# Kernel tuning notes

Measured on AMD Instinct MI355X. Metric: run time of the kernel, lower is better.

Reference implementation:

```python
import jax, jax.numpy as jnp
import numpy as np

B, C, H, W = 8, 4, 96, 96
HW = H * W
DIST = 320.0 ** 2  # ctor default normalizer
INF = 1e10


def _edge_mask(img, pad_val):
    # img: [H, W]. 4-neighbor sum with out-of-bounds value pad_val
    # (pad_val=1 for background channel 0, else 0), matching torch F.pad usage.
    row = jnp.full((1, W), pad_val, img.dtype)
    col = jnp.full((H, 1), pad_val, img.dtype)
    below = jnp.concatenate([img[1:, :], row], axis=0)   # neighbor below
    above = jnp.concatenate([row, img[:-1, :]], axis=0)  # neighbor above
    right = jnp.concatenate([img[:, 1:], col], axis=1)   # neighbor right
    left = jnp.concatenate([col, img[:, :-1]], axis=1)   # neighbor left
    edge = jnp.clip(4.0 * img - (below + above + right + left), 0.0, 1.0)
    return edge > 0  # nonzero() selection as boolean mask over pixels


def _pairwise_sqdist_table():
    # D[p, g] = squared euclidean distance between pixel coords p and g. [HW, HW]
    dy = (jnp.arange(H, dtype=jnp.float32)[:, None] - jnp.arange(H, dtype=jnp.float32)[None, :]) ** 2
    dx = (jnp.arange(W, dtype=jnp.float32)[:, None] - jnp.arange(W, dtype=jnp.float32)[None, :]) ** 2
    return (dy[:, None, :, None] + dx[None, :, None, :]).reshape(HW, HW)


def setup_inputs() -> dict:
    key = jax.random.key(0)
    k1, k2 = jax.random.split(key)
    pred = jax.random.randint(k1, (B, C, H, W), 0, 2).astype(jnp.float32)
    GT = jax.random.randint(k2, (B, C, H, W), 0, 2).astype(jnp.float32)
    return {"pred": pred, "GT": GT}


def reference(pred, GT):
    pad_vals = jnp.where(jnp.arange(C) == 0, 1.0, 0.0).astype(pred.dtype)  # channel 0 pads with 1
    edge_fn = jax.vmap(jax.vmap(_edge_mask, in_axes=(0, 0)), in_axes=(0, None))  # over B then C
    pm = edge_fn(pred, pad_vals).reshape(B * C, HW)  # pred edge masks
    gm = edge_fn(GT, pad_vals).reshape(B * C, HW)    # GT edge masks

    D = _pairwise_sqdist_table()  # [HW, HW], shared across all (b, c)

    def one_pair(masks):
        p, g = masks
        # min over GT edge pixels of squared distance, for every pixel. [HW]
        minvals = jnp.min(jnp.where(g[None, :], D, INF), axis=1)
        # directed Hausdorff: max over pred edge pixels (mins are >= 0, so 0 sentinel is safe)
        val = jnp.max(jnp.where(p, minvals, 0.0))
        # original skips (leaves 0) when either edge set is empty
        return jnp.where(jnp.any(p) & jnp.any(g), val, 0.0)

    vals = jax.lax.map(one_pair, (pm, gm))  # sequential over B*C to bound memory
    return jnp.sum(vals) / DIST
```

## Files before the change

kernel.cpp:

```cpp
#include <hip/hip_runtime.h>

#define HDIM 96
#define WDIM 96
#define HWSZ (HDIM * WDIM)
#define NPAIRS 32
#define NONE_DIST 1000
#define NONE_D 1000000
#define DIST_NORM 102400.0f

__device__ __forceinline__ int nsb96(unsigned long long lo, unsigned long long hi, int y) {
    unsigned long long a, b;
    if (y == 0)      { a = lo;                                b = hi; }
    else if (y < 64) { a = (lo >> y) | (hi << (64 - y));      b = hi >> y; }
    else             { a = hi >> (y - 64);                    b = 0ull; }
    if (a) return (int)__ffsll(a) - 1;
    if (b) return 64 + (int)__ffsll(b) - 1;
    return NONE_DIST;
}

__global__ __launch_bounds__(1024) void hausdorff_fused_kernel(
    const float* __restrict__ pred, const float* __restrict__ GT,
    int* __restrict__ ws ,
    float* __restrict__ out) {
    const int pair = blockIdx.x;
    const int padi = ((pair & 3) == 0) ? 1 : 0;
    const float* __restrict__ P = pred + (size_t)pair * HWSZ;
    const float* __restrict__ G = GT + (size_t)pair * HWSZ;

    __shared__ int GbT[WDIM * (HDIM + 1)];
    __shared__ unsigned char Pb[HWSZ];
    __shared__ int d1[HWSZ];
    __shared__ unsigned long long c_lo[WDIM], c_hi[WDIM];
    __shared__ unsigned long long r_lo[WDIM], r_hi[WDIM];
    __shared__ int wmax[16], wflag[16];

    const int tid = threadIdx.x;
    const int lane = tid & 63;
    const int wv = tid >> 6;

    for (int k = 0; k < 9; ++k) {
        const int i = tid + (k << 10);
        const int y = i / WDIM, x = i - y * WDIM;
        Pb[i] = (P[i] != 0.0f);
        GbT[x * 97 + y] = (G[i] != 0.0f);
    }
    __syncthreads();

    int ganyw = 0;
    for (int x = wv; x < WDIM; x += 16) {
        int e0;
        {
            const int y = lane;
            const int c  = GbT[x * 97 + y];
            const int dn = GbT[x * 97 + y + 1];
            const int up = (y > 0)        ? GbT[x * 97 + y - 1] : padi;
            const int rt = (x + 1 < WDIM) ? GbT[(x + 1) * 97 + y] : padi;
            const int lt = (x > 0)        ? GbT[(x - 1) * 97 + y] : padi;
            e0 = (4 * c - (dn + up + rt + lt)) > 0;
        }
        const unsigned long long lo = __ballot(e0);
        int e1 = 0;
        if (lane < 32) {
            const int y = 64 + lane;
            const int c  = GbT[x * 97 + y];
            const int dn = (y + 1 < HDIM) ? GbT[x * 97 + y + 1] : padi;
            const int up = GbT[x * 97 + y - 1];
            const int rt = (x + 1 < WDIM) ? GbT[(x + 1) * 97 + y] : padi;
            const int lt = (x > 0)        ? GbT[(x - 1) * 97 + y] : padi;
            e1 = (4 * c - (dn + up + rt + lt)) > 0;
        }
        const unsigned long long hi = __ballot(e1) & 0xffffffffull;
        ganyw |= ((lo | hi) != 0ull);
        if (lane == 0) {
            c_lo[x] = lo;
            c_hi[x] = hi;
            const unsigned long long rl = __brevll(hi), rh = __brevll(lo);
            r_lo[x] = (rl >> 32) | (rh << 32);
            r_hi[x] = rh >> 32;
        }
    }
    __syncthreads();

    for (int k = 0; k < 9; ++k) {
        const int i = tid + (k << 10);
        const int y = i / WDIM, x = i - y * WDIM;
        const int dd = nsb96(c_lo[x], c_hi[x], y);
        const int du = nsb96(r_lo[x], r_hi[x], 95 - y);
        const int n = min(dd, du);
        d1[i] = (n >= NONE_DIST) ? NONE_D : n * n;
    }
    __syncthreads();

    int bestMax = 0;
    int anyP = 0;
    for (int k = 0; k < 9; ++k) {
        const int i = tid + (k << 10);
        const int y = i / WDIM, x = i - y * WDIM;
        const int c  = Pb[i];
        const int dn = (y + 1 < HDIM) ? Pb[i + WDIM] : padi;
        const int up = (y > 0)        ? Pb[i - WDIM] : padi;
        const int rt = (x + 1 < WDIM) ? Pb[i + 1]    : padi;
        const int lt = (x > 0)        ? Pb[i - 1]    : padi;
        const int pm = (4 * c - (dn + up + rt + lt)) > 0;
        anyP |= pm;
        if (pm) {
            int best = d1[i];
            for (int r = 1; r < WDIM; ++r) {
                const int rr = r * r;
                if (rr >= best) break;
                if (x - r >= 0)   best = min(best, d1[i - r] + rr);
                if (x + r < WDIM) best = min(best, d1[i + r] + rr);
            }
            bestMax = max(bestMax, best);
        }
    }

    for (int off = 32; off > 0; off >>= 1) {
        bestMax = max(bestMax, __shfl_down(bestMax, off));
        anyP |= __shfl_down(anyP, off);
    }
    if (lane == 0) {
        wmax[wv] = bestMax;
        wflag[wv] = ((anyP ? 1 : 0) << 1) | (ganyw ? 1 : 0);
    }
    __syncthreads();

    if (tid == 0) {
        int m = 0, fP = 0, fG = 0;
        for (int w = 0; w < 16; ++w) {
            m = max(m, wmax[w]);
            fP |= (wflag[w] >> 1) & 1;
            fG |= wflag[w] & 1;
        }
        const int val = (fP && fG) ? m : 0;
        atomicAdd(&ws[0], val);
        __threadfence();
        const int old = atomicAdd(&ws[1], 1);
        if (old == NPAIRS - 1) {
            __threadfence();
            const int total = atomicAdd(&ws[0], 0);
            out[0] = (float)total / DIST_NORM;
        }
    }
}

extern "C" void kernel_launch(void* const* d_in, const int* in_sizes, int n_in,
                              void* d_out, int out_size, void* d_ws, size_t ws_size,
                              hipStream_t stream) {
    const float* pred = (const float*)d_in[0];
    const float* GT = (const float*)d_in[1];
    float* out = (float*)d_out;
    int* ws = (int*)d_ws;

    hipMemsetAsync(ws, 0, 2 * sizeof(int), stream);
    hausdorff_fused_kernel<<<NPAIRS, 1024, 0, stream>>>(pred, GT, ws, out);
}
```

Measured before the change: 68.76 us.

## Pack binary masks into column bitmasks and compute edges with bitwise ops

Loads pred and GT as float4 and packs them into byte-packed words in shared memory. It then builds per-column 96-bit occupancy masks with ballots and computes the edge masks of both images using bitwise neighbour shifts, replacing per-pixel 4-neighbour sums. The main distance loop now tests the precomputed pred edge bit instead of recomputing the edge from byte loads, and it skips that loop entirely when either edge set is empty. This adds an extra barrier phase, and the shared-memory flags are written without atomics, which is benign here.

```diff
diff --git a/kernel.cpp b/kernel.cpp
--- a/kernel.cpp
+++ b/kernel.cpp
@@ -2,11 +2,11 @@
 
 #define HDIM 96
 #define WDIM 96
-#define HWSZ (HDIM * WDIM)
+#define HWSZ 9216
 #define NPAIRS 32
-#define NONE_DIST 1000
 #define NONE_D 1000000
 #define DIST_NORM 102400.0f
+#define RSTRIDE 25
 
 __device__ __forceinline__ int nsb96(unsigned long long lo, unsigned long long hi, int y) {
     unsigned long long a, b;
@@ -15,7 +15,7 @@
     else             { a = hi >> (y - 64);                    b = 0ull; }
     if (a) return (int)__ffsll(a) - 1;
     if (b) return 64 + (int)__ffsll(b) - 1;
-    return NONE_DIST;
+    return 1000;
 }
 
 __global__ __launch_bounds__(1024) void hausdorff_fused_kernel(
@@ -24,59 +24,83 @@
     float* __restrict__ out) {
     const int pair = blockIdx.x;
     const int padi = ((pair & 3) == 0) ? 1 : 0;
-    const float* __restrict__ P = pred + (size_t)pair * HWSZ;
-    const float* __restrict__ G = GT + (size_t)pair * HWSZ;
+    const float4* __restrict__ P4 = (const float4*)(pred + (size_t)pair * HWSZ);
+    const float4* __restrict__ G4 = (const float4*)(GT + (size_t)pair * HWSZ);
 
-    __shared__ int GbT[WDIM * (HDIM + 1)];
-    __shared__ unsigned char Pb[HWSZ];
+    __shared__ unsigned int PbW[HDIM * RSTRIDE];
+    __shared__ unsigned int GbW[HDIM * RSTRIDE];
+    __shared__ unsigned long long Pc_lo[96], Pc_hi[96];
+    __shared__ unsigned long long Gc_lo[96], Gc_hi[96];
+    __shared__ unsigned long long EP_lo[96], EP_hi[96];
+    __shared__ unsigned long long EG_lo[96], EG_hi[96];
+    __shared__ unsigned long long RG_lo[96], RG_hi[96];
     __shared__ int d1[HWSZ];
-    __shared__ unsigned long long c_lo[WDIM], c_hi[WDIM];
-    __shared__ unsigned long long r_lo[WDIM], r_hi[WDIM];
-    __shared__ int wmax[16], wflag[16];
+    __shared__ int wmax[16];
+    __shared__ int sAnyP, sAnyG;
 
     const int tid = threadIdx.x;
     const int lane = tid & 63;
     const int wv = tid >> 6;
+    if (tid == 0) { sAnyP = 0; sAnyG = 0; }
 
-    for (int k = 0; k < 9; ++k) {
-        const int i = tid + (k << 10);
-        const int y = i / WDIM, x = i - y * WDIM;
-        Pb[i] = (P[i] != 0.0f);
-        GbT[x * 97 + y] = (G[i] != 0.0f);
+    for (int q = tid; q < 2304; q += 1024) {
+        const int y = q / 24, xq = q - y * 24;
+        const float4 p = P4[q], g = G4[q];
+        const unsigned int pw = (p.x != 0.f ? 1u : 0u) | (p.y != 0.f ? 1u << 8 : 0u) |
+                                (p.z != 0.f ? 1u << 16 : 0u) | (p.w != 0.f ? 1u << 24 : 0u);
+        const unsigned int gw = (g.x != 0.f ? 1u : 0u) | (g.y != 0.f ? 1u << 8 : 0u) |
+                                (g.z != 0.f ? 1u << 16 : 0u) | (g.w != 0.f ? 1u << 24 : 0u);
+        PbW[y * RSTRIDE + xq] = pw;
+        GbW[y * RSTRIDE + xq] = gw;
     }
     __syncthreads();
 
-    int ganyw = 0;
-    for (int x = wv; x < WDIM; x += 16) {
-        int e0;
-        {
-            const int y = lane;
-            const int c  = GbT[x * 97 + y];
-            const int dn = GbT[x * 97 + y + 1];
-            const int up = (y > 0)        ? GbT[x * 97 + y - 1] : padi;
-            const int rt = (x + 1 < WDIM) ? GbT[(x + 1) * 97 + y] : padi;
-            const int lt = (x > 0)        ? GbT[(x - 1) * 97 + y] : padi;
-            e0 = (4 * c - (dn + up + rt + lt)) > 0;
+    for (int x = 6 * wv; x < 6 * wv + 6; ++x) {
+        const int xw = x >> 2, sh = (x & 3) * 8;
+        const int pb = (PbW[lane * RSTRIDE + xw] >> sh) & 1;
+        const int gb = (GbW[lane * RSTRIDE + xw] >> sh) & 1;
+        const unsigned long long plo = __ballot(pb);
+        const unsigned long long glo = __ballot(gb);
+        int pbh = 0, gbh = 0;
+        if (lane < 32) {
+            pbh = (PbW[(64 + lane) * RSTRIDE + xw] >> sh) & 1;
+            gbh = (GbW[(64 + lane) * RSTRIDE + xw] >> sh) & 1;
         }
-        const unsigned long long lo = __ballot(e0);
-        int e1 = 0;
-        if (lane < 32) {
-            const int y = 64 + lane;
-            const int c  = GbT[x * 97 + y];
-            const int dn = (y + 1 < HDIM) ? GbT[x * 97 + y + 1] : padi;
-            const int up = GbT[x * 97 + y - 1];
-            const int rt = (x + 1 < WDIM) ? GbT[(x + 1) * 97 + y] : padi;
-            const int lt = (x > 0)        ? GbT[(x - 1) * 97 + y] : padi;
-            e1 = (4 * c - (dn + up + rt + lt)) > 0;
+        const unsigned long long phi = __ballot(pbh) & 0xffffffffull;
+        const unsigned long long ghi = __ballot(gbh) & 0xffffffffull;
+        if (lane == 0) {
+            Pc_lo[x] = plo; Pc_hi[x] = phi;
+            Gc_lo[x] = glo; Gc_hi[x] = ghi;
         }
-        const unsigned long long hi = __ballot(e1) & 0xffffffffull;
-        ganyw |= ((lo | hi) != 0ull);
-        if (lane == 0) {
-            c_lo[x] = lo;
-            c_hi[x] = hi;
-            const unsigned long long rl = __brevll(hi), rh = __brevll(lo);
-            r_lo[x] = (rl >> 32) | (rh << 32);
-            r_hi[x] = rh >> 32;
+    }
+    __syncthreads();
+
+    if (tid < 96 || (tid >= 128 && tid < 224)) {
+        const bool isP = (tid < 96);
+        const int x = isP ? tid : tid - 128;
+        const unsigned long long* Clo = isP ? Pc_lo : Gc_lo;
+        const unsigned long long* Chi = isP ? Pc_hi : Gc_hi;
+        const unsigned long long clo = Clo[x], chi = Chi[x];
+        const unsigned long long ulo = (clo << 1) | (unsigned long long)padi;
+        const unsigned long long uhi = ((chi << 1) | (clo >> 63)) & 0xffffffffull;
+        const unsigned long long dlo = (clo >> 1) | (chi << 63);
+        const unsigned long long dhi = (chi >> 1) | ((unsigned long long)padi << 31);
+        unsigned long long llo, lhi, rlo, rhi;
+        if (x > 0)  { llo = Clo[x - 1]; lhi = Chi[x - 1]; }
+        else        { llo = padi ? ~0ull : 0ull; lhi = padi ? 0xffffffffull : 0ull; }
+        if (x < 95) { rlo = Clo[x + 1]; rhi = Chi[x + 1]; }
+        else        { rlo = padi ? ~0ull : 0ull; rhi = padi ? 0xffffffffull : 0ull; }
+        const unsigned long long elo = clo & ~(ulo & dlo & llo & rlo);
+        const unsigned long long ehi = (chi & ~(uhi & dhi & lhi & rhi)) & 0xffffffffull;
+        if (isP) {
+            EP_lo[x] = elo; EP_hi[x] = ehi;
+            if (elo | ehi) sAnyP = 1;
+        } else {
+            EG_lo[x] = elo; EG_hi[x] = ehi;
+            const unsigned long long rl = __brevll(ehi), rh = __brevll(elo);
+            RG_lo[x] = (rl >> 32) | (rh << 32);
+            RG_hi[x] = rh >> 32;
+            if (elo | ehi) sAnyG = 1;
         }
     }
     __syncthreads();
@@ -84,55 +108,42 @@
     for (int k = 0; k < 9; ++k) {
         const int i = tid + (k << 10);
         const int y = i / WDIM, x = i - y * WDIM;
-        const int dd = nsb96(c_lo[x], c_hi[x], y);
-        const int du = nsb96(r_lo[x], r_hi[x], 95 - y);
+        const int dd = nsb96(EG_lo[x], EG_hi[x], y);
+        const int du = nsb96(RG_lo[x], RG_hi[x], 95 - y);
         const int n = min(dd, du);
-        d1[i] = (n >= NONE_DIST) ? NONE_D : n * n;
+        d1[i] = (n >= 1000) ? NONE_D : n * n;
     }
     __syncthreads();
 
     int bestMax = 0;
-    int anyP = 0;
-    for (int k = 0; k < 9; ++k) {
-        const int i = tid + (k << 10);
-        const int y = i / WDIM, x = i - y * WDIM;
-        const int c  = Pb[i];
-        const int dn = (y + 1 < HDIM) ? Pb[i + WDIM] : padi;
-        const int up = (y > 0)        ? Pb[i - WDIM] : padi;
-        const int rt = (x + 1 < WDIM) ? Pb[i + 1]    : padi;
-        const int lt = (x > 0)        ? Pb[i - 1]    : padi;
-        const int pm = (4 * c - (dn + up + rt + lt)) > 0;
-        anyP |= pm;
-        if (pm) {
-            int best = d1[i];
-            for (int r = 1; r < WDIM; ++r) {
-                const int rr = r * r;
-                if (rr >= best) break;
-                if (x - r >= 0)   best = min(best, d1[i - r] + rr);
-                if (x + r < WDIM) best = min(best, d1[i + r] + rr);
+    const bool live = (sAnyP != 0) && (sAnyG != 0);
+    if (live) {
+        for (int k = 0; k < 9; ++k) {
+            const int i = tid + (k << 10);
+            const int y = i / WDIM, x = i - y * WDIM;
+            const unsigned long long ep = (y < 64) ? EP_lo[x] : EP_hi[x];
+            if ((ep >> (y & 63)) & 1) {
+                int best = d1[i];
+                for (int r = 1; r < WDIM; ++r) {
+                    const int rr = r * r;
+                    if (rr >= best) break;
+                    if (x - r >= 0)   best = min(best, d1[i - r] + rr);
+                    if (x + r < WDIM) best = min(best, d1[i + r] + rr);
+                }
+                bestMax = max(bestMax, best);
             }
-            bestMax = max(bestMax, best);
         }
     }
 
-    for (int off = 32; off > 0; off >>= 1) {
+    for (int off = 32; off > 0; off >>= 1)
         bestMax = max(bestMax, __shfl_down(bestMax, off));
-        anyP |= __shfl_down(anyP, off);
-    }
-    if (lane == 0) {
-        wmax[wv] = bestMax;
-        wflag[wv] = ((anyP ? 1 : 0) << 1) | (ganyw ? 1 : 0);
-    }
+    if (lane == 0) wmax[wv] = bestMax;
     __syncthreads();
 
     if (tid == 0) {
-        int m = 0, fP = 0, fG = 0;
-        for (int w = 0; w < 16; ++w) {
-            m = max(m, wmax[w]);
-            fP |= (wflag[w] >> 1) & 1;
-            fG |= wflag[w] & 1;
-        }
-        const int val = (fP && fG) ? m : 0;
+        int m = 0;
+        for (int w = 0; w < 16; ++w) m = max(m, wmax[w]);
+        const int val = live ? m : 0;
         atomicAdd(&ws[0], val);
         __threadfence();
         const int old = atomicAdd(&ws[1], 1);
```

Result: faster. 66.77 us (-2.9%).
